# Kernel tuning notes

Measured on AMD Instinct MI355X. Metric: run time of the kernel, lower is better.

Reference implementation:

```python
import jax, jax.numpy as jnp
import numpy as np

B, N, D, H = 4, 2048, 1024, 16
HD = D // H
SCALE = HD ** -0.5

def neg_softmax(x):
    # sign(x) * softmax(|x|) along last axis
    return jnp.sign(x) * jax.nn.softmax(jnp.abs(x), axis=-1)

def setup_inputs() -> dict:
    key = jax.random.key(0)
    ks = jax.random.split(key, 9)
    s = 0.02
    return {
        "x": jax.random.normal(ks[0], (B, N, D), jnp.float32),
        "Wq": jax.random.normal(ks[1], (D, D), jnp.float32) * s,
        "bq": jax.random.normal(ks[2], (D,), jnp.float32) * s,
        "Wk": jax.random.normal(ks[3], (D, D), jnp.float32) * s,
        "bk": jax.random.normal(ks[4], (D,), jnp.float32) * s,
        "Wv": jax.random.normal(ks[5], (D, D), jnp.float32) * s,
        "bv": jax.random.normal(ks[6], (D,), jnp.float32) * s,
        "Wo": jax.random.normal(ks[7], (D, D), jnp.float32) * s,
        "bo": jax.random.normal(ks[8], (D,), jnp.float32) * s,
    }

def reference(x, Wq, bq, Wk, bk, Wv, bv, Wo, bo):
    def heads(t):  # [B,N,D] -> [B,H,N,hd]
        return t.reshape(B, N, H, HD).transpose(0, 2, 1, 3)
    Q = heads(x @ Wq.T + bq)
    K = heads(x @ Wk.T + bk)
    V = heads(x @ Wv.T + bv)
    logits = jnp.einsum('bhnd,bhmd->bhnm', Q, K) * SCALE
    attn = neg_softmax(logits)
    out = jnp.einsum('bhnm,bhmd->bhnd', attn, V)
    out = out.transpose(0, 2, 1, 3).reshape(B, N, D)
    return out @ Wo.T + bo
```

## Files before the change

kernel.cpp:

```cpp
#include <hip/hip_runtime.h>

typedef _Float16 f16x8 __attribute__((ext_vector_type(8)));
typedef __fp16 h16x2 __attribute__((ext_vector_type(2)));
typedef float f32x4 __attribute__((ext_vector_type(4)));
typedef unsigned short u16x4 __attribute__((ext_vector_type(4)));

#define NB 4
#define NSEQ 2048
#define NH 16
#define HDIM 64
#define DM 1024
#define MROWS (NB * NSEQ)

#define AS1 __attribute__((address_space(1)))
#define AS3 __attribute__((address_space(3)))

__device__ __forceinline__ float exp2_fast(float x) {
  float r; asm("v_exp_f32 %0, %1" : "=v"(r) : "v"(x)); return r;
}

__device__ __forceinline__ unsigned short f2h(float f) {
  _Float16 h = (_Float16)f;
  union { _Float16 h; unsigned short u; } v; v.h = h;
  return v.u;
}

__global__ void cvt_all_kernel(const float* __restrict__ x, const float* __restrict__ w0,
                               const float* __restrict__ w1, const float* __restrict__ w2,
                               const float* __restrict__ w3, unsigned short* __restrict__ xo,
                               unsigned short* __restrict__ o0, unsigned short* __restrict__ o1,
                               unsigned short* __restrict__ o2, unsigned short* __restrict__ o3) {
  const int id = blockIdx.x * blockDim.x + threadIdx.x;
  const float* src; unsigned short* dst; int i;
  if (id < (MROWS * DM) / 4) { src = x; dst = xo; i = id; }
  else {
    const int id2 = id - (MROWS * DM) / 4;
    const int w = id2 >> 18;
    i = id2 & 262143;
    switch (w) {
      case 0: src = w0; dst = o0; break;
      case 1: src = w1; dst = o1; break;
      case 2: src = w2; dst = o2; break;
      default: src = w3; dst = o3; break;
    }
  }
  const float4 v = ((const float4*)src)[i];
  u16x4 o;
  o.x = f2h(v.x); o.y = f2h(v.y); o.z = f2h(v.z); o.w = f2h(v.w);
  ((u16x4*)dst)[i] = o;
}

template<int OUT_F16>
__device__ __forceinline__
void gemm_body(const unsigned short* __restrict__ A, const unsigned short* __restrict__ Bw,
               const float* __restrict__ bias, void* __restrict__ Cv, float scale,
               unsigned short* As, unsigned short* Bs) {
  const int tid = threadIdx.x, lane = tid & 63, wave = tid >> 6;
  const int g = lane >> 4, c = lane & 15;
  const int orig = blockIdx.y * 8 + blockIdx.x;
  const int wg = (orig & 7) * 64 + (orig >> 3);
  const int m0 = (wg >> 3) * 128, n0 = (wg & 7) * 128;
  const int wm = (wave >> 1) * 64, wn = (wave & 1) * 64;
  f32x4 acc[4][4] = {};
  for (int kt = 0; kt < 1024; kt += 32) {
#pragma unroll
    for (int p = 0; p < 2; ++p) {
      const int idx = p * 256 + tid;
      const int row = idx >> 2, col = (idx & 3) * 8;
      __builtin_amdgcn_global_load_lds(
          (const AS1 void*)(A + (size_t)(m0 + row) * 1024 + kt + col),
          (AS3 void*)(As + idx * 8), 16, 0, 0);
      __builtin_amdgcn_global_load_lds(
          (const AS1 void*)(Bw + (size_t)(n0 + row) * 1024 + kt + col),
          (AS3 void*)(Bs + idx * 8), 16, 0, 0);
    }
    __syncthreads();
    f16x8 af[4], bfr[4];
#pragma unroll
    for (int i = 0; i < 4; ++i) af[i] = *(const f16x8*)(As + (wm + i * 16 + c) * 32 + g * 8);
#pragma unroll
    for (int i = 0; i < 4; ++i) bfr[i] = *(const f16x8*)(Bs + (wn + i * 16 + c) * 32 + g * 8);
#pragma unroll
    for (int i = 0; i < 4; ++i)
#pragma unroll
      for (int j = 0; j < 4; ++j)
        acc[i][j] = __builtin_amdgcn_mfma_f32_16x16x32_f16(af[i], bfr[j], acc[i][j], 0, 0, 0);
    __syncthreads();
  }
#pragma unroll
  for (int i = 0; i < 4; ++i)
#pragma unroll
    for (int j = 0; j < 4; ++j)
#pragma unroll
      for (int r = 0; r < 4; ++r) {
        const int row = m0 + wm + i * 16 + g * 4 + r;
        const int col = n0 + wn + j * 16 + c;
        const float v = (acc[i][j][r] + bias[col]) * scale;
        if (OUT_F16) ((unsigned short*)Cv)[(size_t)row * 1024 + col] = f2h(v);
        else         ((float*)Cv)[(size_t)row * 1024 + col] = v;
      }
}

__global__ __launch_bounds__(256)
void gemm_qkv(const unsigned short* __restrict__ A,
              const unsigned short* __restrict__ W0, const unsigned short* __restrict__ W1,
              const unsigned short* __restrict__ W2,
              const float* __restrict__ b0, const float* __restrict__ b1,
              const float* __restrict__ b2,
              unsigned short* __restrict__ C0, unsigned short* __restrict__ C1,
              unsigned short* __restrict__ C2, float qscale) {
  __shared__ unsigned short As[128 * 32];
  __shared__ unsigned short Bs[128 * 32];
  const unsigned short* Bw; const float* bias; unsigned short* C; float scale;
  switch (blockIdx.z) {
    case 0:  Bw = W0; bias = b0; C = C0; scale = qscale; break;
    case 1:  Bw = W1; bias = b1; C = C1; scale = 1.f; break;
    default: Bw = W2; bias = b2; C = C2; scale = 1.f; break;
  }
  gemm_body<1>(A, Bw, bias, C, scale, As, Bs);
}

__global__ __launch_bounds__(256)
void gemm_out(const unsigned short* __restrict__ A, const unsigned short* __restrict__ Bw,
              const float* __restrict__ bias, float* __restrict__ Cv) {
  __shared__ unsigned short As[128 * 32];
  __shared__ unsigned short Bs[128 * 32];
  gemm_body<0>(A, Bw, bias, Cv, 1.f, As, Bs);
}

__global__ __launch_bounds__(256, 2)
void attn_kernel(const unsigned short* __restrict__ Qg, const unsigned short* __restrict__ Kg,
                 const unsigned short* __restrict__ Vg, unsigned short* __restrict__ Og) {
  __shared__ __align__(16) unsigned short Kl[2][64 * 64];
  __shared__ __align__(16) unsigned short Vt[2][64 * 72];
  const int tid = threadIdx.x, lane = tid & 63, wave = tid >> 6;
  const int g = lane >> 4, c = lane & 15;
  const int orig = blockIdx.y * 8 + blockIdx.x;
  const int wg = (orig & 7) * 64 + (orig >> 3);
  const int qblk = wg & 7, bh = wg >> 3;
  const int b = bh >> 4, h = bh & 15;
  const int q0 = qblk * 256 + wave * 64;
  const size_t rb = (size_t)b * NSEQ;
  const int hc = h * HDIM;
  const int NT = NSEQ / 64;

  const int k_kvo = tid >> 3;
  const int k_d   = (((tid & 7) ^ ((tid >> 3) & 7)) * 8);
  const int v_i = tid & 31;
  const int v_ds8 = (tid >> 5) * 8;
  const int v_r0 = 2 * v_i;
  const int pv2 = (v_r0 & 32) | (((v_r0 >> 2) & 3) << 3) | (((v_r0 >> 4) & 1) << 2) | (v_r0 & 3);

  f16x8 qf[4][2];
#pragma unroll
  for (int m = 0; m < 4; ++m)
#pragma unroll
    for (int kb2 = 0; kb2 < 2; ++kb2)
      qf[m][kb2] = *(const f16x8*)(Qg + (rb + q0 + m * 16 + c) * DM + hc + kb2 * 32 + g * 8);

  f32x4 oT[4][4] = {};
  float dpart[4] = {0.f, 0.f, 0.f, 0.f};
  f16x8 vreg[2];

  auto stageK = [&](int t, int buf) {
    const int kv0 = t * 64;
#pragma unroll
    for (int p = 0; p < 2; ++p) {
      const int kv = kv0 + 32 * p + k_kvo;
      __builtin_amdgcn_global_load_lds(
          (const AS1 void*)(Kg + (rb + kv) * DM + hc + k_d),
          (AS3 void*)(&Kl[buf][p * 2048 + tid * 8]), 16, 0, 0);
    }
  };
  auto loadV = [&](int t) {
    const unsigned short* src = Vg + (rb + t * 64 + v_r0) * DM + hc + v_ds8;
    vreg[0] = *(const f16x8*)(src);
    vreg[1] = *(const f16x8*)(src + DM);
  };
  auto writeV = [&](int buf) {
    union { f16x8 v; unsigned short u[8]; } a, bb;
    a.v = vreg[0]; bb.v = vreg[1];
#pragma unroll
    for (int j = 0; j < 8; ++j) {
      union { unsigned short s[2]; unsigned u; } w;
      w.s[0] = a.u[j]; w.s[1] = bb.u[j];
      *(unsigned*)(&Vt[buf][(v_ds8 + j) * 72 + pv2]) = w.u;
    }
  };

  stageK(0, 0);
  loadV(0);
  writeV(0);
  __syncthreads();

  for (int t = 0; t < NT; ++t) {
    const int cur = t & 1;
    if (t + 1 < NT) { stageK(t + 1, cur ^ 1); loadV(t + 1); }

    const unsigned short* KL = Kl[cur];
    const unsigned short* VT = Vt[cur];

    f16x8 kf[2][4];
#pragma unroll
    for (int kb2 = 0; kb2 < 2; ++kb2)
#pragma unroll
      for (int nb = 0; nb < 4; ++nb)
        kf[kb2][nb] = *(const f16x8*)(KL + (nb * 16 + c) * 64 + (((kb2 * 32 + g * 8) ^ ((c & 7) * 8))));
    f16x8 vtf[2][4];
#pragma unroll
    for (int kb2 = 0; kb2 < 2; ++kb2)
#pragma unroll
      for (int db = 0; db < 4; ++db)
        vtf[kb2][db] = *(const f16x8*)(VT + (db * 16 + c) * 72 + kb2 * 32 + g * 8);

#pragma unroll
    for (int m = 0; m < 4; ++m) {
      f32x4 s[4] = {};
      __builtin_amdgcn_s_setprio(1);
#pragma unroll
      for (int nb = 0; nb < 4; ++nb)
#pragma unroll
        for (int kb2 = 0; kb2 < 2; ++kb2)
          s[nb] = __builtin_amdgcn_mfma_f32_16x16x32_f16(kf[kb2][nb], qf[m][kb2], s[nb], 0, 0, 0);
      __builtin_amdgcn_s_setprio(0);

      union PW { f16x8 v; h16x2 w[4]; } pf[2];
      float es0 = 0.f, es1 = 0.f;
#pragma unroll
      for (int nb = 0; nb < 4; ++nb) {
        float p[4];
#pragma unroll
        for (int r = 0; r < 4; ++r) {
          const float sv = s[nb][r];
          const float e = exp2_fast(fabsf(sv) - 18.0f);
          if (r & 1) es1 += e; else es0 += e;
          p[r] = copysignf(e, sv);
        }
        pf[nb >> 1].w[(nb & 1) * 2]     = __builtin_amdgcn_cvt_pkrtz(p[0], p[1]);
        pf[nb >> 1].w[(nb & 1) * 2 + 1] = __builtin_amdgcn_cvt_pkrtz(p[2], p[3]);
      }
      dpart[m] += es0 + es1;

      __builtin_amdgcn_s_setprio(1);
#pragma unroll
      for (int db = 0; db < 4; ++db) {
        oT[db][m] = __builtin_amdgcn_mfma_f32_16x16x32_f16(vtf[0][db], pf[0].v, oT[db][m], 0, 0, 0);
        oT[db][m] = __builtin_amdgcn_mfma_f32_16x16x32_f16(vtf[1][db], pf[1].v, oT[db][m], 0, 0, 0);
      }
      __builtin_amdgcn_s_setprio(0);
    }

    if (t + 1 < NT) writeV(cur ^ 1);
    __syncthreads();
  }

#pragma unroll
  for (int m = 0; m < 4; ++m) {
    float d = dpart[m];
    d += __shfl_xor(d, 16);
    d += __shfl_xor(d, 32);
    const float inv = 1.f / d;
#pragma unroll
    for (int db = 0; db < 4; ++db) {
      h16x2 h01 = __builtin_amdgcn_cvt_pkrtz(oT[db][m][0] * inv, oT[db][m][1] * inv);
      h16x2 h23 = __builtin_amdgcn_cvt_pkrtz(oT[db][m][2] * inv, oT[db][m][3] * inv);
      union { h16x2 h; unsigned u; } a, bb; a.h = h01; bb.h = h23;
      union { uint2 u2; unsigned u[2]; } st;
      st.u[0] = a.u; st.u[1] = bb.u;
      *(uint2*)(Og + (rb + q0 + m * 16 + c) * DM + hc + db * 16 + g * 4) = st.u2;
    }
  }
}

extern "C" void kernel_launch(void* const* d_in, const int* in_sizes, int n_in,
                              void* d_out, int out_size, void* d_ws, size_t ws_size,
                              hipStream_t stream) {
  const float* x  = (const float*)d_in[0];
  const float* Wq = (const float*)d_in[1];
  const float* bq = (const float*)d_in[2];
  const float* Wk = (const float*)d_in[3];
  const float* bk = (const float*)d_in[4];
  const float* Wv = (const float*)d_in[5];
  const float* bv = (const float*)d_in[6];
  const float* Wo = (const float*)d_in[7];
  const float* bo = (const float*)d_in[8];
  float* out = (float*)d_out;

  unsigned short* xb  = (unsigned short*)d_ws;
  unsigned short* wqb = xb  + (size_t)MROWS * DM;
  unsigned short* wkb = wqb + (size_t)DM * DM;
  unsigned short* wvb = wkb + (size_t)DM * DM;
  unsigned short* wob = wvb + (size_t)DM * DM;
  unsigned short* qb  = wob + (size_t)DM * DM;
  unsigned short* kb  = qb  + (size_t)MROWS * DM;
  unsigned short* vb  = kb  + (size_t)MROWS * DM;
  unsigned short* ab  = xb;

  cvt_all_kernel<<<(MROWS * DM / 4 + 4 * DM * DM / 4) / 256, 256, 0, stream>>>(
      x, Wq, Wk, Wv, Wo, xb, wqb, wkb, wvb, wob);

  const float SC = 0.125f * 1.4426950408889634f;
  gemm_qkv<<<dim3(DM / 128, MROWS / 128, 3), 256, 0, stream>>>(
      xb, wqb, wkb, wvb, bq, bk, bv, qb, kb, vb, SC);

  attn_kernel<<<dim3(NSEQ / 256, NB * NH), 256, 0, stream>>>(qb, kb, vb, ab);

  gemm_out<<<dim3(DM / 128, MROWS / 128), 256, 0, stream>>>(ab, wob, bo, out);
}
```

Measured before the change: 194.0 us.

## Process 128-key tiles per barrier with split V staging in attention

The attention loop now stages 128 KV rows per iteration, computing two 64-row sub-tiles between barriers. This halves the number of __syncthreads calls and interleaves the V global loads and LDS writes for the second half with compute on the first. The s_setprio hints around the MFMA blocks are also removed. LDS use per block doubles to roughly 70 KB, which may limit the two-blocks-per-CU occupancy target.

```diff
diff --git a/kernel.cpp b/kernel.cpp
--- a/kernel.cpp
+++ b/kernel.cpp
@@ -131,8 +131,8 @@
 __global__ __launch_bounds__(256, 2)
 void attn_kernel(const unsigned short* __restrict__ Qg, const unsigned short* __restrict__ Kg,
                  const unsigned short* __restrict__ Vg, unsigned short* __restrict__ Og) {
-  __shared__ __align__(16) unsigned short Kl[2][64 * 64];
-  __shared__ __align__(16) unsigned short Vt[2][64 * 72];
+  __shared__ __align__(16) unsigned short Kl[2][2 * 64 * 64];
+  __shared__ __align__(16) unsigned short Vt[2][2 * 64 * 72];
   const int tid = threadIdx.x, lane = tid & 63, wave = tid >> 6;
   const int g = lane >> 4, c = lane & 15;
   const int orig = blockIdx.y * 8 + blockIdx.x;
@@ -142,7 +142,7 @@
   const int q0 = qblk * 256 + wave * 64;
   const size_t rb = (size_t)b * NSEQ;
   const int hc = h * HDIM;
-  const int NT = NSEQ / 64;
+  const int NT2 = NSEQ / 128;
 
   const int k_kvo = tid >> 3;
   const int k_d   = (((tid & 7) ^ ((tid >> 3) & 7)) * 8);
@@ -163,43 +163,32 @@
   f16x8 vreg[2];
 
   auto stageK = [&](int t, int buf) {
-    const int kv0 = t * 64;
-#pragma unroll
-    for (int p = 0; p < 2; ++p) {
-      const int kv = kv0 + 32 * p + k_kvo;
+#pragma unroll
+    for (int p = 0; p < 4; ++p) {
+      const int kv = t * 128 + 32 * p + k_kvo;
       __builtin_amdgcn_global_load_lds(
           (const AS1 void*)(Kg + (rb + kv) * DM + hc + k_d),
           (AS3 void*)(&Kl[buf][p * 2048 + tid * 8]), 16, 0, 0);
     }
   };
-  auto loadV = [&](int t) {
-    const unsigned short* src = Vg + (rb + t * 64 + v_r0) * DM + hc + v_ds8;
+  auto loadV = [&](int t, int sub) {
+    const unsigned short* src = Vg + (rb + t * 128 + sub * 64 + v_r0) * DM + hc + v_ds8;
     vreg[0] = *(const f16x8*)(src);
     vreg[1] = *(const f16x8*)(src + DM);
   };
-  auto writeV = [&](int buf) {
+  auto writeV = [&](int buf, int sub) {
+    unsigned short* base = &Vt[buf][sub * 4608];
     union { f16x8 v; unsigned short u[8]; } a, bb;
     a.v = vreg[0]; bb.v = vreg[1];
 #pragma unroll
     for (int j = 0; j < 8; ++j) {
       union { unsigned short s[2]; unsigned u; } w;
       w.s[0] = a.u[j]; w.s[1] = bb.u[j];
-      *(unsigned*)(&Vt[buf][(v_ds8 + j) * 72 + pv2]) = w.u;
+      *(unsigned*)(base + (v_ds8 + j) * 72 + pv2) = w.u;
     }
   };
 
-  stageK(0, 0);
-  loadV(0);
-  writeV(0);
-  __syncthreads();
-
-  for (int t = 0; t < NT; ++t) {
-    const int cur = t & 1;
-    if (t + 1 < NT) { stageK(t + 1, cur ^ 1); loadV(t + 1); }
-
-    const unsigned short* KL = Kl[cur];
-    const unsigned short* VT = Vt[cur];
-
+  auto compute_sub = [&](const unsigned short* KL, const unsigned short* VT) {
     f16x8 kf[2][4];
 #pragma unroll
     for (int kb2 = 0; kb2 < 2; ++kb2)
@@ -216,13 +205,11 @@
 #pragma unroll
     for (int m = 0; m < 4; ++m) {
       f32x4 s[4] = {};
-      __builtin_amdgcn_s_setprio(1);
 #pragma unroll
       for (int nb = 0; nb < 4; ++nb)
 #pragma unroll
         for (int kb2 = 0; kb2 < 2; ++kb2)
           s[nb] = __builtin_amdgcn_mfma_f32_16x16x32_f16(kf[kb2][nb], qf[m][kb2], s[nb], 0, 0, 0);
-      __builtin_amdgcn_s_setprio(0);
 
       union PW { f16x8 v; h16x2 w[4]; } pf[2];
       float es0 = 0.f, es1 = 0.f;
@@ -241,16 +228,32 @@
       }
       dpart[m] += es0 + es1;
 
-      __builtin_amdgcn_s_setprio(1);
 #pragma unroll
       for (int db = 0; db < 4; ++db) {
         oT[db][m] = __builtin_amdgcn_mfma_f32_16x16x32_f16(vtf[0][db], pf[0].v, oT[db][m], 0, 0, 0);
         oT[db][m] = __builtin_amdgcn_mfma_f32_16x16x32_f16(vtf[1][db], pf[1].v, oT[db][m], 0, 0, 0);
       }
-      __builtin_amdgcn_s_setprio(0);
-    }
-
-    if (t + 1 < NT) writeV(cur ^ 1);
+    }
+  };
+
+  stageK(0, 0);
+  loadV(0, 0); writeV(0, 0);
+  loadV(0, 1); writeV(0, 1);
+  __syncthreads();
+
+  for (int t = 0; t < NT2; ++t) {
+    const int cur = t & 1;
+    const int nxt = cur ^ 1;
+    const bool more = (t + 1 < NT2);
+    if (more) { stageK(t + 1, nxt); loadV(t + 1, 0); }
+
+    compute_sub(&Kl[cur][0], &Vt[cur][0]);
+
+    if (more) { writeV(nxt, 0); loadV(t + 1, 1); }
+
+    compute_sub(&Kl[cur][4096], &Vt[cur][4608]);
+
+    if (more) writeV(nxt, 1);
     __syncthreads();
   }
 
```

After: 334.7 us. 1.72x slower.
